# Performance work log

Measured on AMD Instinct MI355X. Metric: run time of the kernel, lower is better.

Reference implementation:

```python
import jax, jax.numpy as jnp
import numpy as np

B, D, F, E, G = 2048, 1024, 4096, 16, 2
EPS = 1e-9
LN_EPS = 1e-5


def setup_inputs() -> dict:
    key = jax.random.key(0)
    ks = jax.random.split(key, 10)
    s_in = 1.0 / np.sqrt(D)
    s_out = 1.0 / np.sqrt(F)
    return {
        "cycle_curve_data": jax.random.normal(ks[0], (B, D), jnp.float32),
        "logits": jax.random.normal(ks[1], (B, E), jnp.float32),
        "moe_masks": jax.random.randint(ks[2], (B, E), 0, 2, jnp.int32),
        "ew_in": jax.random.uniform(ks[3], (E, D, F), jnp.float32, -s_in, s_in),
        "ew_out": jax.random.uniform(ks[4], (E, F, D), jnp.float32, -s_out, s_out),
        "eb_out": jax.random.uniform(ks[5], (E, D), jnp.float32, -s_out, s_out),
        "gw_in": jax.random.uniform(ks[6], (G, D, F), jnp.float32, -s_in, s_in),
        "gw_out": jax.random.uniform(ks[7], (G, F, D), jnp.float32, -s_out, s_out),
        "gb_out": jax.random.uniform(ks[8], (G, D), jnp.float32, -s_out, s_out),
        "ln_gamma": jnp.ones((D,), jnp.float32),
        "ln_beta": jnp.zeros((D,), jnp.float32),
    }


def _moe_forward(x, logits, moe_masks, ew_in, ew_out, eb_out, gw_in, gw_out, gb_out, ln_gamma, ln_beta):
    b = x.shape[0]
    mask = (moe_masks == 1).astype(logits.dtype)          # [B,E]
    raw = jax.nn.softmax(logits, axis=1)                   # [B,E]
    gates = raw * mask
    gates = gates / (jnp.sum(gates, axis=1, keepdims=True) + EPS)
    # Per-expert MLPBlockGELU over all tokens; gate=0 zeroes out non-dispatched
    # tokens exactly as MOEDispatcher.combine does.
    h = jax.nn.gelu(jnp.einsum('bd,edf->ebf', x, ew_in), approximate=False)  # [E,B,F]
    eout = jnp.einsum('ebf,efd->ebd', h, ew_out) + eb_out[:, None, :]        # [E,B,D]
    moe_out = jnp.einsum('be,ebd->bd', gates, eout).astype(jnp.bfloat16)     # combine + bf16 cast
    # general experts (dense, added to routed output; bf16+f32 promotes to f32)
    gh = jax.nn.gelu(jnp.einsum('bd,gdf->gbf', x, gw_in), approximate=False)
    gout = jnp.einsum('gbf,gfd->gbd', gh, gw_out) + gb_out[:, None, :]       # [G,B,D]
    final = jnp.sum(gout, axis=0) + moe_out                                  # f32
    # residual + LayerNorm
    y = final + x
    mu = jnp.mean(y, axis=-1, keepdims=True)
    var = jnp.mean(jnp.square(y - mu), axis=-1, keepdims=True)
    final_out = (y - mu) * jax.lax.rsqrt(var + LN_EPS) * ln_gamma + ln_beta
    # training losses
    expert_logits = jnp.mean(raw, axis=0)                                    # [E]
    expert_sample_count = jnp.sum((gates != 0).astype(raw.dtype), axis=0) / b
    aug_loss = jnp.mean(expert_logits * expert_sample_count)
    s = jnp.sum(raw * mask) / b
    guide_loss = (1.0 - s) * (1.0 - s)
    return final_out, aug_loss, guide_loss


def reference(cycle_curve_data, logits, moe_masks, ew_in, ew_out, eb_out, gw_in, gw_out, gb_out, ln_gamma, ln_beta):
    return _moe_forward(cycle_curve_data, logits, moe_masks, ew_in, ew_out, eb_out,
                        gw_in, gw_out, gb_out, ln_gamma, ln_beta)
```

## Files before the change

### kernel.cpp

```cpp
#include <hip/hip_runtime.h>
#include <hip/hip_bf16.h>

#define B_TOK 2048
#define DDIM 1024
#define FDIM 4096
#define NE 16
#define NG 2
#define BD ((long)B_TOK * DDIM)

typedef unsigned short u16;
typedef __attribute__((ext_vector_type(8))) short bf16x8;
typedef __attribute__((ext_vector_type(4))) float f32x4;

__device__ inline u16 f2bf(float x) {
  union { float f; unsigned u; } v; v.f = x;
  return (u16)((v.u + 0x7fffu + ((v.u >> 16) & 1u)) >> 16);
}
__device__ inline float bfround(float x) {
  union { float f; unsigned u; } v; v.f = x;
  v.u = ((v.u + 0x7fffu + ((v.u >> 16) & 1u)) >> 16) << 16;
  return v.f;
}
__device__ inline float fast_erf(float x) {
  float ax = fabsf(x);
  float t = __builtin_amdgcn_rcpf(1.0f + 0.3275911f * ax);
  float poly = t * (0.254829592f + t * (-0.284496736f + t * (1.421413741f +
               t * (-1.453152027f + t * 1.061405429f))));
  float r = 1.0f - poly * __expf(-ax * ax);
  return copysignf(r, x);
}
__device__ inline float gelu_exact(float x) {
  return 0.5f * x * (1.0f + fast_erf(x * 0.70710678118654752440f));
}
__device__ inline void gload16(const void* g, void* l) {
  __builtin_amdgcn_global_load_lds((const __attribute__((address_space(1))) void*)g,
                                   (__attribute__((address_space(3))) void*)l, 16, 0, 0);
}
__device__ inline float waveSum(float v) {
  v += __shfl_down(v, 32); v += __shfl_down(v, 16); v += __shfl_down(v, 8);
  v += __shfl_down(v, 4);  v += __shfl_down(v, 2);  v += __shfl_down(v, 1);
  return v;
}

__global__ __launch_bounds__(256) void gating_kernel(
    const float* __restrict__ logits, const int* __restrict__ masks,
    float* __restrict__ gates, float* __restrict__ loss)
{
  const int b = blockIdx.x * 256 + threadIdx.x;
  const int lane = threadIdx.x & 63;
  const float* lr = logits + (long)b * NE;
  const int*   mr = masks  + (long)b * NE;
  float raw[NE]; int mk[NE];
  float mx = -1e30f;
#pragma unroll
  for (int e = 0; e < NE; ++e) { raw[e] = lr[e]; mx = fmaxf(mx, raw[e]); }
  float s = 0.f;
#pragma unroll
  for (int e = 0; e < NE; ++e) { raw[e] = expf(raw[e] - mx); s += raw[e]; }
  float inv = 1.0f / s;
#pragma unroll
  for (int e = 0; e < NE; ++e) raw[e] *= inv;
  float gs = 0.f;
#pragma unroll
  for (int e = 0; e < NE; ++e) { mk[e] = (mr[e] == 1); gs += mk[e] ? raw[e] : 0.f; }
  float ginv = 1.0f / (gs + 1e-9f);
  float* gr = gates + (long)b * NE;
#pragma unroll
  for (int e = 0; e < NE; ++e) gr[e] = (mk[e] ? raw[e] : 0.f) * ginv;
#pragma unroll
  for (int e = 0; e < NE; ++e) {
    float cs = waveSum(raw[e]);
    float cc = waveSum(mk[e] ? 1.f : 0.f);
    if (lane == 0) { atomicAdd(&loss[e], cs); atomicAdd(&loss[NE + e], cc); }
  }
  float t = waveSum(gs);
  if (lane == 0) atomicAdd(&loss[32], t);
}

__global__ void finalize_loss(const float* __restrict__ loss, float* __restrict__ out2) {
  if (threadIdx.x == 0) {
    float aug = 0.f;
    for (int e = 0; e < NE; ++e)
      aug += (loss[e] / (float)B_TOK) * (loss[NE + e] / (float)B_TOK);
    aug *= (1.0f / NE);
    float s = loss[32] / (float)B_TOK;
    out2[0] = aug;
    out2[1] = (1.f - s) * (1.f - s);
  }
}

__global__ __launch_bounds__(256) void compact_kernel(
    const int* __restrict__ masks, int* __restrict__ tok,
    int* __restrict__ pos, int* __restrict__ cnts)
{
  const int e = blockIdx.x, tid = threadIdx.x;
  const int lane = tid & 63, wave = tid >> 6;
  __shared__ int wcnt[4];
  __shared__ int runbase;
  if (tid == 0) runbase = 0;
  __syncthreads();
  for (int b0 = 0; b0 < B_TOK; b0 += 256) {
    int b = b0 + tid;
    int m = (masks[(long)b * NE + e] == 1);
    unsigned long long bal = __ballot(m);
    int pre = __popcll(bal & ((1ull << lane) - 1ull));
    if (lane == 0) wcnt[wave] = __popcll(bal);
    __syncthreads();
    int base = runbase;
    for (int w = 0; w < wave; ++w) base += wcnt[w];
    if (m) {
      int p = base + pre;
      tok[(e << 11) + p] = b;
      pos[(long)b * NE + e] = p;
    } else {
      pos[(long)b * NE + e] = -1;
    }
    __syncthreads();
    if (tid == 0) runbase += wcnt[0] + wcnt[1] + wcnt[2] + wcnt[3];
    __syncthreads();
  }
  const int cnt = runbase;
  const int cnt_pad = (cnt + 127) & ~127;
  for (int i = cnt + tid; i < cnt_pad; i += 256)
    tok[(e << 11) + i] = 0;
  if (tid == 0) { cnts[e] = cnt; cnts[NE + e] = cnt_pad; }
}

__global__ __launch_bounds__(256) void cvt_x_kernel(const float* __restrict__ x, u16* __restrict__ xb) {
  long i = ((long)blockIdx.x * 256 + threadIdx.x) * 4;
  float4 v = *(const float4*)&x[i];
  ushort4 o; o.x = f2bf(v.x); o.y = f2bf(v.y); o.z = f2bf(v.z); o.w = f2bf(v.w);
  *(ushort4*)&xb[i] = o;
}

__global__ __launch_bounds__(256) void bias_init_kernel(
    const float* __restrict__ gates, const float* __restrict__ eb,
    float* __restrict__ moe_bias)
{
  long i = (long)blockIdx.x * 256 + threadIdx.x;
  int b = (int)(i >> 10), d = (int)(i & 1023);
  const float* gr = gates + (long)b * NE;
  float s = 0.f;
#pragma unroll
  for (int e = 0; e < NE; ++e) s += gr[e] * eb[e * DDIM + d];
  moe_bias[i] = s;
}

__global__ __launch_bounds__(256) void transpose_cvt(
    const float* __restrict__ src, u16* __restrict__ dst,
    int R, int C, long sZ, long dZ)
{
  __shared__ float t[64][65];
  const float* s = src + (long)blockIdx.z * sZ;
  u16* d = dst + (long)blockIdx.z * dZ;
  const int c0 = blockIdx.x * 64, r0 = blockIdx.y * 64;
  const int tid = threadIdx.x;
#pragma unroll
  for (int it = 0; it < 4; ++it) {
    int idx = tid + it * 256;
    int r = idx >> 4, cq = (idx & 15) * 4;
    float4 v = *(const float4*)&s[(long)(r0 + r) * C + c0 + cq];
    t[r][cq] = v.x; t[r][cq + 1] = v.y; t[r][cq + 2] = v.z; t[r][cq + 3] = v.w;
  }
  __syncthreads();
#pragma unroll
  for (int it = 0; it < 4; ++it) {
    int idx = tid + it * 256;
    int c = idx >> 4, rq = (idx & 15) * 4;
    ushort4 o;
    o.x = f2bf(t[rq][c]); o.y = f2bf(t[rq+1][c]); o.z = f2bf(t[rq+2][c]); o.w = f2bf(t[rq+3][c]);
    *(ushort4*)&d[(long)(c0 + c) * R + r0 + rq] = o;
  }
}

template<int MODE>
__global__ __launch_bounds__(256) void gemm128(
    const u16* __restrict__ A, int lda, long aZ,
    const u16* __restrict__ Bm, int ldb, long bZ,
    int klen,
    u16* __restrict__ H, long hZ,
    float* __restrict__ C, long cZ,
    const int* __restrict__ tok, const int* __restrict__ cnts, int ebase)
{
  int lin = ((int)blockIdx.z * gridDim.y + blockIdx.y) * gridDim.x + blockIdx.x;
  const int T = gridDim.x * gridDim.y * gridDim.z;
  lin = (lin & 7) * (T >> 3) + (lin >> 3);
  const int PZ = gridDim.x * gridDim.y;
  const int bz = lin / PZ;
  const int r  = lin - bz * PZ;
  const int nSx = gridDim.x >> 2;
  const int st = r >> 4, pos = r & 15;
  const int bx = ((st % nSx) << 2) + (pos & 3);
  const int by = ((st / nSx) << 2) + (pos >> 2);

  const int zi = (MODE == 2) ? (bz >> 2) : bz;
  const int ks = (MODE == 2) ? (bz & 3) * klen : 0;
  const int m0 = by * 128, n0 = bx * 128;
  if (MODE != 2 && cnts && m0 >= cnts[NE + ebase + zi]) return;

  __shared__ u16 sA[3][128 * 32];
  __shared__ u16 sB[3][128 * 32];
  const u16* Az = A + (long)zi * aZ;
  const u16* Bz = Bm + (long)zi * bZ;
  const int tid = threadIdx.x, lane = tid & 63, wave = tid >> 6;

  const int off = tid * 16;
  const int sr  = off >> 6;
  const int ske = (off & 63) >> 1;
  int arow0 = m0 + sr, arow1 = m0 + sr + 64;
  if (MODE == 0 && tok) {
    const int* tz = tok + ((ebase + zi) << 11);
    arow0 = tz[arow0]; arow1 = tz[arow1];
  }
  const u16* gA0 = Az + (long)arow0 * lda + ks + ske;
  const u16* gA1 = Az + (long)arow1 * lda + ks + ske;
  const u16* gB0 = Bz + (long)(n0 + sr) * ldb + ks + ske;
  const u16* gB1 = Bz + (long)(n0 + sr + 64) * ldb + ks + ske;

  const int wr = wave >> 1, wc = wave & 1;
  const int fr = lane & 15, fk = (lane >> 4) * 8;
  const int rAo = (wr * 64 + fr) * 32 + fk;
  const int rBo = (wc * 64 + fr) * 32 + fk;

  f32x4 zero = {0.f, 0.f, 0.f, 0.f};
  f32x4 acc[4][4];
#pragma unroll
  for (int m = 0; m < 4; ++m)
#pragma unroll
    for (int n = 0; n < 4; ++n) acc[m][n] = zero;

  auto STAGE = [&](u16* dA, u16* dB, int t) {
    const int kk = t << 5;
    gload16(gA0 + kk, dA + wave * 512);
    gload16(gA1 + kk, dA + 2048 + wave * 512);
    gload16(gB0 + kk, dB + wave * 512);
    gload16(gB1 + kk, dB + 2048 + wave * 512);
  };
  auto COMPUTE = [&](const u16* bA, const u16* bB) {
    bf16x8 av[4], bv[4];
#pragma unroll
    for (int m = 0; m < 4; ++m) av[m] = *(const bf16x8*)(bA + rAo + m * 512);
#pragma unroll
    for (int n = 0; n < 4; ++n) bv[n] = *(const bf16x8*)(bB + rBo + n * 512);
#pragma unroll
    for (int m = 0; m < 4; ++m)
#pragma unroll
      for (int n = 0; n < 4; ++n)
        acc[m][n] = __builtin_amdgcn_mfma_f32_16x16x32_bf16(av[m], bv[n], acc[m][n], 0, 0, 0);
  };

#define PIPE(SA, SB, KIDX, CA, CB)                                   \
  STAGE(SA, SB, KIDX);                                               \
  asm volatile("s_waitcnt vmcnt(8)" ::: "memory");                   \
  __builtin_amdgcn_s_barrier();                                      \
  asm volatile("" ::: "memory");                                     \
  COMPUTE(CA, CB);                                                   \
  asm volatile("" ::: "memory");                                     \
  __builtin_amdgcn_s_barrier();                                      \
  asm volatile("" ::: "memory");

  const int nt = klen >> 5;
  STAGE(sA[0], sB[0], 0);
  STAGE(sA[1], sB[1], 1);
  for (int t = 0; t + 2 < nt; t += 3) {
    PIPE(sA[2], sB[2], t + 2, sA[0], sB[0]);
    PIPE(sA[0], sB[0], t + 3, sA[1], sB[1]);
    PIPE(sA[1], sB[1], t + 4, sA[2], sB[2]);
  }
  asm volatile("s_waitcnt vmcnt(4)" ::: "memory");
  __builtin_amdgcn_s_barrier();
  asm volatile("" ::: "memory");
  COMPUTE(sA[0], sB[0]);
  asm volatile("s_waitcnt vmcnt(0)" ::: "memory");
  __builtin_amdgcn_s_barrier();
  asm volatile("" ::: "memory");
  COMPUTE(sA[1], sB[1]);
#undef PIPE

  const int er = m0 + wr * 64 + (lane >> 4) * 4;
  const int ec = n0 + wc * 64 + fr;
  if (MODE == 0) {
    u16* Hz = H + (long)zi * hZ;
#pragma unroll
    for (int m = 0; m < 4; ++m)
#pragma unroll
      for (int n = 0; n < 4; ++n) {
        f32x4 v = acc[m][n];
        int rb = er + m * 16, cb = ec + n * 16;
#pragma unroll
        for (int j = 0; j < 4; ++j)
          Hz[(long)(rb + j) * FDIM + cb] = f2bf(gelu_exact(v[j]));
      }
  } else if (MODE == 1) {
    float* Cz = C + (long)(ebase + zi) * cZ;
#pragma unroll
    for (int m = 0; m < 4; ++m)
#pragma unroll
      for (int n = 0; n < 4; ++n) {
        f32x4 v = acc[m][n];
        int rb = er + m * 16, cb = ec + n * 16;
#pragma unroll
        for (int j = 0; j < 4; ++j)
          Cz[(long)(rb + j) * DDIM + cb] = v[j];
      }
  } else {
    float* Cz = C + (long)bz * cZ;
#pragma unroll
    for (int m = 0; m < 4; ++m)
#pragma unroll
      for (int n = 0; n < 4; ++n) {
        f32x4 v = acc[m][n];
        int rb = er + m * 16, cb = ec + n * 16;
#pragma unroll
        for (int j = 0; j < 4; ++j)
          Cz[(long)(rb + j) * DDIM + cb] = v[j];
      }
  }
}

__global__ __launch_bounds__(256) void combine_ln_kernel(
    const float* __restrict__ x, const float* __restrict__ moe_bias,
    const float* __restrict__ Eout, const float* __restrict__ gen_p,
    const float* __restrict__ gb,
    const int* __restrict__ pos, const float* __restrict__ gates,
    const float* __restrict__ gamma, const float* __restrict__ beta,
    float* __restrict__ out)
{
  const int b = blockIdx.x, tid = threadIdx.x;
  const int lane = tid & 63, wave = tid >> 6;
  const long base = (long)b * DDIM;
  __shared__ int posr[NE];
  __shared__ float gr[NE];
  __shared__ float red[4];
  if (tid < NE) { posr[tid] = pos[(long)b * NE + tid]; gr[tid] = gates[(long)b * NE + tid]; }
  __syncthreads();
  float y[4];
  float ls = 0.f;
#pragma unroll
  for (int i = 0; i < 4; ++i) {
    int d = tid + i * 256;
    long idx = base + d;
    float moe = moe_bias[idx];
#pragma unroll
    for (int e = 0; e < NE; ++e) {
      int p = posr[e];
      if (p >= 0) moe += gr[e] * Eout[((long)e * B_TOK + p) * DDIM + d];
    }
    moe = bfround(moe);
    float ge = gb[d] + gb[DDIM + d];
#pragma unroll
    for (int sl = 0; sl < 8; ++sl) ge += gen_p[(long)sl * BD + idx];
    y[i] = moe + ge + x[idx];
    ls += y[i];
  }
  float t = waveSum(ls);
  if (lane == 0) red[wave] = t;
  __syncthreads();
  float mean = (red[0] + red[1] + red[2] + red[3]) * (1.0f / DDIM);
  __syncthreads();
  float vs = 0.f;
#pragma unroll
  for (int i = 0; i < 4; ++i) { float d2 = y[i] - mean; vs += d2 * d2; }
  t = waveSum(vs);
  if (lane == 0) red[wave] = t;
  __syncthreads();
  float var = (red[0] + red[1] + red[2] + red[3]) * (1.0f / DDIM);
  float inv = rsqrtf(var + 1e-5f);
#pragma unroll
  for (int i = 0; i < 4; ++i) {
    int d = tid + i * 256;
    out[base + d] = (y[i] - mean) * inv * gamma[d] + beta[d];
  }
}

extern "C" void kernel_launch(void* const* d_in, const int* in_sizes, int n_in,
                              void* d_out, int out_size, void* d_ws, size_t ws_size,
                              hipStream_t stream)
{
  const float* x      = (const float*)d_in[0];
  const float* logits = (const float*)d_in[1];
  const int*   masks  = (const int*)d_in[2];
  const float* ew_in  = (const float*)d_in[3];
  const float* ew_out = (const float*)d_in[4];
  const float* eb_out = (const float*)d_in[5];
  const float* gw_in  = (const float*)d_in[6];
  const float* gw_out = (const float*)d_in[7];
  const float* gb_out = (const float*)d_in[8];
  const float* gamma  = (const float*)d_in[9];
  const float* beta   = (const float*)d_in[10];
  float* out = (float*)d_out;

  char* w = (char*)d_ws;
  size_t off = 0;
  auto alloc = [&](size_t bytes) -> void* {
    off = (off + 4095) & ~(size_t)4095;
    void* p = w + off; off += bytes; return p;
  };
  const long DF = (long)DDIM * FDIM;
  const long BF = (long)B_TOK * FDIM;

  float* gates    = (float*)alloc((size_t)B_TOK * NE * 4);
  float* loss     = (float*)alloc(64 * 4);
  int*   tok      = (int*)alloc((size_t)NE * B_TOK * 4);
  int*   pos      = (int*)alloc((size_t)B_TOK * NE * 4);
  int*   cnts     = (int*)alloc(2 * NE * 4);
  u16*   xb       = (u16*)alloc((size_t)BD * 2);
  float* moe_bias = (float*)alloc((size_t)BD * 4);
  float* gen_p    = (float*)alloc(8 * (size_t)BD * 4);
  float* Eout     = (float*)alloc((size_t)NE * BD * 4);

  const size_t per = 2 * (size_t)DF * 2 + (size_t)BF * 2 + 3 * 4096;
  int CE = 16;
  while (CE > 1 && off + (size_t)CE * per > ws_size) CE >>= 1;
  u16* WinT  = (u16*)alloc((size_t)CE * DF * 2);
  u16* WoutT = (u16*)alloc((size_t)CE * DF * 2);
  u16* Hb    = (u16*)alloc((size_t)CE * BF * 2);

  hipMemsetAsync(loss, 0, 64 * 4, stream);
  gating_kernel<<<8, 256, 0, stream>>>(logits, masks, gates, loss);
  finalize_loss<<<1, 64, 0, stream>>>(loss, out + BD);
  compact_kernel<<<NE, 256, 0, stream>>>(masks, tok, pos, cnts);
  cvt_x_kernel<<<2048, 256, 0, stream>>>(x, xb);
  bias_init_kernel<<<8192, 256, 0, stream>>>(gates, eb_out, moe_bias);

  for (int e0 = 0; e0 < NE; e0 += CE) {
    transpose_cvt<<<dim3(FDIM/64, DDIM/64, CE), 256, 0, stream>>>(
        ew_in + (long)e0 * DF, WinT, DDIM, FDIM, DF, DF);
    transpose_cvt<<<dim3(DDIM/64, FDIM/64, CE), 256, 0, stream>>>(
        ew_out + (long)e0 * DF, WoutT, FDIM, DDIM, DF, DF);
    gemm128<0><<<dim3(FDIM/128, B_TOK/128, CE), 256, 0, stream>>>(
        xb, DDIM, 0L, WinT, DDIM, DF, DDIM,
        Hb, BF, nullptr, 0L, tok, cnts, e0);
    gemm128<1><<<dim3(DDIM/128, B_TOK/128, CE), 256, 0, stream>>>(
        Hb, FDIM, BF, WoutT, FDIM, DF, FDIM,
        nullptr, 0L, Eout, BD, nullptr, cnts, e0);
  }

  transpose_cvt<<<dim3(FDIM/64, DDIM/64, NG), 256, 0, stream>>>(
      gw_in, WinT, DDIM, FDIM, DF, DF);
  transpose_cvt<<<dim3(DDIM/64, FDIM/64, NG), 256, 0, stream>>>(
      gw_out, WoutT, FDIM, DDIM, DF, DF);
  gemm128<0><<<dim3(FDIM/128, B_TOK/128, NG), 256, 0, stream>>>(
      xb, DDIM, 0L, WinT, DDIM, DF, DDIM,
      Hb, BF, nullptr, 0L, nullptr, nullptr, 0);
  gemm128<2><<<dim3(DDIM/128, B_TOK/128, NG * 4), 256, 0, stream>>>(
      Hb, FDIM, BF, WoutT, FDIM, DF, FDIM / 4,
      nullptr, 0L, gen_p, BD, nullptr, nullptr, 0);

  combine_ln_kernel<<<B_TOK, 256, 0, stream>>>(
      x, moe_bias, Eout, gen_p, gb_out, pos, gates, gamma, beta, out);
}
```

Measured before the change: 763.3 us.

## Replace 128x128 GEMM with 256x128 eight-wave pipelined kernel using swizzled LDS

Replaces the 4-wave 128x128x32 GEMM with an 8-wave 256x128x64 tile kernel. It uses XOR-swizzled LDS to avoid bank conflicts, interleaves global staging with four MFMA phases per K step, and raises wave priority around the MFMA phases. Expert token padding grows to 256 to match the larger M tile, and the general-expert split-K drops from 4 to 2 slices, which halves the partial buffers the combine kernel reads. The larger tiles increase reuse but may waste work on padded rows and lower occupancy.

```diff
diff --git a/kernel.cpp b/kernel.cpp
--- a/kernel.cpp
+++ b/kernel.cpp
@@ -120,7 +120,7 @@
     __syncthreads();
   }
   const int cnt = runbase;
-  const int cnt_pad = (cnt + 127) & ~127;
+  const int cnt_pad = (cnt + 255) & ~255;
   for (int i = cnt + tid; i < cnt_pad; i += 256)
     tok[(e << 11) + i] = 0;
   if (tid == 0) { cnts[e] = cnt; cnts[NE + e] = cnt_pad; }
@@ -174,9 +174,9 @@
 }
 
 template<int MODE>
-__global__ __launch_bounds__(256) void gemm128(
+__global__ __launch_bounds__(512, 2) void gemm8p(
     const u16* __restrict__ A, int lda, long aZ,
-    const u16* __restrict__ Bm, int ldb, long bZ,
+    const u16* __restrict__ Bm, int ldb,
     int klen,
     u16* __restrict__ H, long hZ,
     float* __restrict__ C, long cZ,
@@ -186,131 +186,149 @@
   const int T = gridDim.x * gridDim.y * gridDim.z;
   lin = (lin & 7) * (T >> 3) + (lin >> 3);
   const int PZ = gridDim.x * gridDim.y;
-  const int bz = lin / PZ;
-  const int r  = lin - bz * PZ;
+  const int z = lin / PZ;
+  const int r = lin - z * PZ;
   const int nSx = gridDim.x >> 2;
-  const int st = r >> 4, pos = r & 15;
-  const int bx = ((st % nSx) << 2) + (pos & 3);
-  const int by = ((st / nSx) << 2) + (pos >> 2);
-
-  const int zi = (MODE == 2) ? (bz >> 2) : bz;
-  const int ks = (MODE == 2) ? (bz & 3) * klen : 0;
-  const int m0 = by * 128, n0 = bx * 128;
-  if (MODE != 2 && cnts && m0 >= cnts[NE + ebase + zi]) return;
-
-  __shared__ u16 sA[3][128 * 32];
-  __shared__ u16 sB[3][128 * 32];
-  const u16* Az = A + (long)zi * aZ;
-  const u16* Bz = Bm + (long)zi * bZ;
+  const int st4 = r >> 4, pos = r & 15;
+  const int bx = ((st4 % nSx) << 2) + (pos & 3);
+  const int by = ((st4 / nSx) << 2) + (pos >> 2);
+
+  const int m0 = by * 256, n0 = bx * 128;
+  if (MODE != 2 && cnts && m0 >= cnts[NE + ebase + z]) return;
+
+  __shared__ u16 lds[3][24576];
+
+  const int zb = (MODE == 2) ? (z >> 1) : z;
+  const int ks = (MODE == 2) ? (z & 1) * klen : 0;
+  const u16* Az = A + (long)((MODE == 0) ? 0 : zb) * aZ;
+  const u16* Bz = Bm + (long)zb * ((long)DDIM * FDIM);
+
   const int tid = threadIdx.x, lane = tid & 63, wave = tid >> 6;
-
-  const int off = tid * 16;
-  const int sr  = off >> 6;
-  const int ske = (off & 63) >> 1;
-  int arow0 = m0 + sr, arow1 = m0 + sr + 64;
-  if (MODE == 0 && tok) {
-    const int* tz = tok + ((ebase + zi) << 11);
-    arow0 = tz[arow0]; arow1 = tz[arow1];
-  }
-  const u16* gA0 = Az + (long)arow0 * lda + ks + ske;
-  const u16* gA1 = Az + (long)arow1 * lda + ks + ske;
-  const u16* gB0 = Bz + (long)(n0 + sr) * ldb + ks + ske;
-  const u16* gB1 = Bz + (long)(n0 + sr + 64) * ldb + ks + ske;
-
   const int wr = wave >> 1, wc = wave & 1;
-  const int fr = lane & 15, fk = (lane >> 4) * 8;
-  const int rAo = (wr * 64 + fr) * 32 + fk;
-  const int rBo = (wc * 64 + fr) * 32 + fk;
-
+  const int fr = lane & 15;
+
+  const int srow = wave * 8 + (lane >> 3);
+  const int skey = ((lane & 7) << 3) ^ ((lane >> 3) << 3);
+  const u16* gA[4];
+  const u16* gB[2];
+#pragma unroll
+  for (int c = 0; c < 4; ++c) {
+    int rr = m0 + c * 64 + srow;
+    if (MODE == 0 && tok) rr = tok[((ebase + z) << 11) + rr];
+    gA[c] = Az + (long)rr * lda + ks + skey;
+  }
+#pragma unroll
+  for (int c = 0; c < 2; ++c)
+    gB[c] = Bz + (long)(n0 + c * 64 + srow) * ldb + ks + skey;
+
+  auto stA = [&](int buf, int t, int c) {
+    gload16(gA[c] + (t << 6), &lds[buf][c * 4096 + wave * 512]);
+  };
+  auto stB = [&](int buf, int t, int c) {
+    gload16(gB[c] + (t << 6), &lds[buf][16384 + c * 4096 + wave * 512]);
+  };
+  auto rdA = [&](int buf, int mi, int kh) -> bf16x8 {
+    int row = wr * 64 + mi * 16 + fr;
+    int keff = ((lane >> 4) * 8 + kh * 32) ^ ((fr & 7) << 3);
+    return *(const bf16x8*)(&lds[buf][row * 64 + keff]);
+  };
+  auto rdB = [&](int buf, int ni, int kh) -> bf16x8 {
+    int row = wc * 64 + ni * 16 + fr;
+    int keff = ((lane >> 4) * 8 + kh * 32) ^ ((fr & 7) << 3);
+    return *(const bf16x8*)(&lds[buf][16384 + row * 64 + keff]);
+  };
+
+  f32x4 acc[4][4];
   f32x4 zero = {0.f, 0.f, 0.f, 0.f};
-  f32x4 acc[4][4];
-#pragma unroll
-  for (int m = 0; m < 4; ++m)
-#pragma unroll
-    for (int n = 0; n < 4; ++n) acc[m][n] = zero;
-
-  auto STAGE = [&](u16* dA, u16* dB, int t) {
-    const int kk = t << 5;
-    gload16(gA0 + kk, dA + wave * 512);
-    gload16(gA1 + kk, dA + 2048 + wave * 512);
-    gload16(gB0 + kk, dB + wave * 512);
-    gload16(gB1 + kk, dB + 2048 + wave * 512);
-  };
-  auto COMPUTE = [&](const u16* bA, const u16* bB) {
-    bf16x8 av[4], bv[4];
-#pragma unroll
-    for (int m = 0; m < 4; ++m) av[m] = *(const bf16x8*)(bA + rAo + m * 512);
-#pragma unroll
-    for (int n = 0; n < 4; ++n) bv[n] = *(const bf16x8*)(bB + rBo + n * 512);
-#pragma unroll
-    for (int m = 0; m < 4; ++m)
-#pragma unroll
-      for (int n = 0; n < 4; ++n)
-        acc[m][n] = __builtin_amdgcn_mfma_f32_16x16x32_bf16(av[m], bv[n], acc[m][n], 0, 0, 0);
-  };
-
-#define PIPE(SA, SB, KIDX, CA, CB)                                   \
-  STAGE(SA, SB, KIDX);                                               \
-  asm volatile("s_waitcnt vmcnt(8)" ::: "memory");                   \
-  __builtin_amdgcn_s_barrier();                                      \
-  asm volatile("" ::: "memory");                                     \
-  COMPUTE(CA, CB);                                                   \
-  asm volatile("" ::: "memory");                                     \
-  __builtin_amdgcn_s_barrier();                                      \
-  asm volatile("" ::: "memory");
-
-  const int nt = klen >> 5;
-  STAGE(sA[0], sB[0], 0);
-  STAGE(sA[1], sB[1], 1);
-  for (int t = 0; t + 2 < nt; t += 3) {
-    PIPE(sA[2], sB[2], t + 2, sA[0], sB[0]);
-    PIPE(sA[0], sB[0], t + 3, sA[1], sB[1]);
-    PIPE(sA[1], sB[1], t + 4, sA[2], sB[2]);
-  }
-  asm volatile("s_waitcnt vmcnt(4)" ::: "memory");
+#pragma unroll
+  for (int mi = 0; mi < 4; ++mi)
+#pragma unroll
+    for (int ni = 0; ni < 4; ++ni) acc[mi][ni] = zero;
+
+  const int nt = klen >> 6;
+#pragma unroll
+  for (int c = 0; c < 4; ++c) stA(0, 0, c);
+  stB(0, 0, 0); stB(0, 0, 1);
+#pragma unroll
+  for (int c = 0; c < 4; ++c) stA(1, 1, c);
+  stB(1, 1, 0); stB(1, 1, 1);
+  asm volatile("s_waitcnt vmcnt(6)" ::: "memory");
   __builtin_amdgcn_s_barrier();
   asm volatile("" ::: "memory");
-  COMPUTE(sA[0], sB[0]);
-  asm volatile("s_waitcnt vmcnt(0)" ::: "memory");
+
+#define PH_MFMA(QM, QN)                                                        \
+  __builtin_amdgcn_s_barrier();                                                \
+  __builtin_amdgcn_sched_barrier(0);                                           \
+  __builtin_amdgcn_s_setprio(1);                                               \
+  _Pragma("unroll")                                                            \
+  for (int kh = 0; kh < 2; ++kh)                                               \
+    _Pragma("unroll")                                                          \
+    for (int m2 = 0; m2 < 2; ++m2)                                             \
+      _Pragma("unroll")                                                        \
+      for (int n2 = 0; n2 < 2; ++n2)                                           \
+        acc[QM * 2 + m2][QN * 2 + n2] = __builtin_amdgcn_mfma_f32_16x16x32_bf16( \
+            af[m2][kh], bf[QN * 2 + n2][kh], acc[QM * 2 + m2][QN * 2 + n2], 0, 0, 0); \
+  __builtin_amdgcn_s_setprio(0);                                               \
+  __builtin_amdgcn_sched_barrier(0);                                           \
+  asm volatile("" ::: "memory");                                               \
   __builtin_amdgcn_s_barrier();
-  asm volatile("" ::: "memory");
-  COMPUTE(sA[1], sB[1]);
-#undef PIPE
+
+  int buf = 0;
+  for (int t = 0; t < nt; ++t) {
+    int sb = buf + 2; if (sb >= 3) sb -= 3;
+    const bool stg = (t + 2 < nt);
+    bf16x8 af[2][2], bf[4][2];
+    af[0][0] = rdA(buf, 0, 0); af[0][1] = rdA(buf, 0, 1);
+    af[1][0] = rdA(buf, 1, 0); af[1][1] = rdA(buf, 1, 1);
+    bf[0][0] = rdB(buf, 0, 0); bf[0][1] = rdB(buf, 0, 1);
+    bf[1][0] = rdB(buf, 1, 0); bf[1][1] = rdB(buf, 1, 1);
+    if (stg) { stA(sb, t + 2, 0); stA(sb, t + 2, 1); }
+    asm volatile("" ::: "memory");
+    PH_MFMA(0, 0)
+    bf[2][0] = rdB(buf, 2, 0); bf[2][1] = rdB(buf, 2, 1);
+    bf[3][0] = rdB(buf, 3, 0); bf[3][1] = rdB(buf, 3, 1);
+    if (stg) { stA(sb, t + 2, 2); stA(sb, t + 2, 3); }
+    asm volatile("" ::: "memory");
+    PH_MFMA(0, 1)
+    af[0][0] = rdA(buf, 2, 0); af[0][1] = rdA(buf, 2, 1);
+    af[1][0] = rdA(buf, 3, 0); af[1][1] = rdA(buf, 3, 1);
+    if (stg) stB(sb, t + 2, 0);
+    asm volatile("" ::: "memory");
+    PH_MFMA(1, 0)
+    if (stg) {
+      stB(sb, t + 2, 1);
+      asm volatile("s_waitcnt vmcnt(6)" ::: "memory");
+    } else if (t + 1 < nt) {
+      asm volatile("s_waitcnt vmcnt(0)" ::: "memory");
+    }
+    asm volatile("" ::: "memory");
+    PH_MFMA(1, 1)
+    buf = buf + 1; if (buf >= 3) buf = 0;
+  }
+#undef PH_MFMA
 
   const int er = m0 + wr * 64 + (lane >> 4) * 4;
   const int ec = n0 + wc * 64 + fr;
   if (MODE == 0) {
-    u16* Hz = H + (long)zi * hZ;
-#pragma unroll
-    for (int m = 0; m < 4; ++m)
-#pragma unroll
-      for (int n = 0; n < 4; ++n) {
-        f32x4 v = acc[m][n];
-        int rb = er + m * 16, cb = ec + n * 16;
+    u16* Hz = H + (long)z * hZ;
+#pragma unroll
+    for (int mi = 0; mi < 4; ++mi)
+#pragma unroll
+      for (int ni = 0; ni < 4; ++ni) {
+        f32x4 v = acc[mi][ni];
+        int rb = er + mi * 16, cb = ec + ni * 16;
 #pragma unroll
         for (int j = 0; j < 4; ++j)
           Hz[(long)(rb + j) * FDIM + cb] = f2bf(gelu_exact(v[j]));
       }
-  } else if (MODE == 1) {
-    float* Cz = C + (long)(ebase + zi) * cZ;
-#pragma unroll
-    for (int m = 0; m < 4; ++m)
-#pragma unroll
-      for (int n = 0; n < 4; ++n) {
-        f32x4 v = acc[m][n];
-        int rb = er + m * 16, cb = ec + n * 16;
-#pragma unroll
-        for (int j = 0; j < 4; ++j)
-          Cz[(long)(rb + j) * DDIM + cb] = v[j];
-      }
   } else {
-    float* Cz = C + (long)bz * cZ;
-#pragma unroll
-    for (int m = 0; m < 4; ++m)
-#pragma unroll
-      for (int n = 0; n < 4; ++n) {
-        f32x4 v = acc[m][n];
-        int rb = er + m * 16, cb = ec + n * 16;
+    float* Cz = (MODE == 1) ? (C + (long)(ebase + z) * cZ) : (C + (long)z * cZ);
+#pragma unroll
+    for (int mi = 0; mi < 4; ++mi)
+#pragma unroll
+      for (int ni = 0; ni < 4; ++ni) {
+        f32x4 v = acc[mi][ni];
+        int rb = er + mi * 16, cb = ec + ni * 16;
 #pragma unroll
         for (int j = 0; j < 4; ++j)
           Cz[(long)(rb + j) * DDIM + cb] = v[j];
@@ -349,7 +367,7 @@
     moe = bfround(moe);
     float ge = gb[d] + gb[DDIM + d];
 #pragma unroll
-    for (int sl = 0; sl < 8; ++sl) ge += gen_p[(long)sl * BD + idx];
+    for (int sl = 0; sl < 4; ++sl) ge += gen_p[(long)sl * BD + idx];
     y[i] = moe + ge + x[idx];
     ls += y[i];
   }
@@ -406,7 +424,7 @@
   int*   cnts     = (int*)alloc(2 * NE * 4);
   u16*   xb       = (u16*)alloc((size_t)BD * 2);
   float* moe_bias = (float*)alloc((size_t)BD * 4);
-  float* gen_p    = (float*)alloc(8 * (size_t)BD * 4);
+  float* gen_p    = (float*)alloc(4 * (size_t)BD * 4);
   float* Eout     = (float*)alloc((size_t)NE * BD * 4);
 
   const size_t per = 2 * (size_t)DF * 2 + (size_t)BF * 2 + 3 * 4096;
@@ -428,11 +446,11 @@
         ew_in + (long)e0 * DF, WinT, DDIM, FDIM, DF, DF);
     transpose_cvt<<<dim3(DDIM/64, FDIM/64, CE), 256, 0, stream>>>(
         ew_out + (long)e0 * DF, WoutT, FDIM, DDIM, DF, DF);
-    gemm128<0><<<dim3(FDIM/128, B_TOK/128, CE), 256, 0, stream>>>(
-        xb, DDIM, 0L, WinT, DDIM, DF, DDIM,
+    gemm8p<0><<<dim3(FDIM/128, B_TOK/256, CE), 512, 0, stream>>>(
+        xb, DDIM, 0L, WinT, DDIM, DDIM,
         Hb, BF, nullptr, 0L, tok, cnts, e0);
-    gemm128<1><<<dim3(DDIM/128, B_TOK/128, CE), 256, 0, stream>>>(
-        Hb, FDIM, BF, WoutT, FDIM, DF, FDIM,
+    gemm8p<1><<<dim3(DDIM/128, B_TOK/256, CE), 512, 0, stream>>>(
+        Hb, FDIM, BF, WoutT, FDIM, FDIM,
         nullptr, 0L, Eout, BD, nullptr, cnts, e0);
   }
 
@@ -440,11 +458,11 @@
       gw_in, WinT, DDIM, FDIM, DF, DF);
   transpose_cvt<<<dim3(DDIM/64, FDIM/64, NG), 256, 0, stream>>>(
       gw_out, WoutT, FDIM, DDIM, DF, DF);
-  gemm128<0><<<dim3(FDIM/128, B_TOK/128, NG), 256, 0, stream>>>(
-      xb, DDIM, 0L, WinT, DDIM, DF, DDIM,
+  gemm8p<0><<<dim3(FDIM/128, B_TOK/256, NG), 512, 0, stream>>>(
+      xb, DDIM, 0L, WinT, DDIM, DDIM,
       Hb, BF, nullptr, 0L, nullptr, nullptr, 0);
-  gemm128<2><<<dim3(DDIM/128, B_TOK/128, NG * 4), 256, 0, stream>>>(
-      Hb, FDIM, BF, WoutT, FDIM, DF, FDIM / 4,
+  gemm8p<2><<<dim3(DDIM/128, B_TOK/256, NG * 2), 512, 0, stream>>>(
+      Hb, FDIM, BF, WoutT, FDIM, FDIM / 2,
       nullptr, 0L, gen_p, BD, nullptr, nullptr, 0);
 
   combine_ln_kernel<<<B_TOK, 256, 0, stream>>>(
```

New measurement: 788.9 us. 3.4% more time.
